# Optimization experiments

Measured on AMD Instinct MI355X. Metric: run time of the kernel, lower is better.

## Reference

```python
import jax, jax.numpy as jnp
import numpy as np

D_MODEL = 512
N_LAYERS = 4
VOCAB = 256
SEQ = 2048
BATCH = 8
EPS = 1e-5


def _ln(x, g, b):
    mu = jnp.mean(x, axis=-1, keepdims=True)
    var = jnp.mean(jnp.square(x - mu), axis=-1, keepdims=True)
    return (x - mu) * jax.lax.rsqrt(var + EPS) * g + b


def setup_inputs() -> dict:
    key = jax.random.key(0)
    ks = jax.random.split(key, 16)
    d, dff = D_MODEL, 4 * D_MODEL
    s = 0.02
    inp = {
        "tokens": jax.random.randint(ks[0], (BATCH, SEQ), 0, VOCAB, dtype=jnp.int64),
        "emb": jax.random.normal(ks[1], (VOCAB, d), jnp.float32) * s,
        "W_upd": jax.random.normal(ks[2], (d, d), jnp.float32) * s,
        "b_upd": jnp.zeros((d,), jnp.float32),
        "W_f": jax.random.normal(ks[3], (d, d), jnp.float32) * s,
        "b_f": jnp.zeros((d,), jnp.float32),
        "decay_param": jnp.zeros((1,), jnp.float32),
        "norm_g": jnp.ones((d,), jnp.float32),
        "norm_b": jnp.zeros((d,), jnp.float32),
        "cms_ln_g": jnp.ones((N_LAYERS, d), jnp.float32),
        "cms_ln_b": jnp.zeros((N_LAYERS, d), jnp.float32),
        "cms_W1": jax.random.normal(ks[4], (N_LAYERS, d, dff), jnp.float32) * s,
        "cms_b1": jnp.zeros((N_LAYERS, dff), jnp.float32),
        "cms_W2": jax.random.normal(ks[5], (N_LAYERS, dff, d), jnp.float32) * s,
        "cms_b2": jnp.zeros((N_LAYERS, d), jnp.float32),
        "head_W": jax.random.normal(ks[6], (d, VOCAB), jnp.float32) * s,
        "head_b": jnp.zeros((VOCAB,), jnp.float32),
    }
    return inp


def _fast_memory(x, mask, W_upd, b_upd, W_f, b_f, decay_param):
    # x: (B,S,d), mask: (B,S) float
    decay = jax.nn.sigmoid(decay_param[0])
    u = jnp.einsum("bsd,de->bse", x, W_upd) + b_upd  # precompute updates
    u_t = jnp.swapaxes(u, 0, 1)                        # (S,B,d)
    m_t = jnp.swapaxes(mask, 0, 1)[..., None]          # (S,B,1)

    def step(mem, inp):
        u_i, msk = inp
        new = decay * mem + u_i
        mem = msk * new + (1.0 - msk) * mem
        return mem, mem

    mem0 = jnp.zeros((x.shape[0], x.shape[2]), x.dtype)
    _, mems = jax.lax.scan(step, mem0, (u_t, m_t))     # (S,B,d)
    mems = jnp.swapaxes(mems, 0, 1)                    # (B,S,d)
    return jnp.einsum("bsd,de->bse", mems, W_f) + b_f


def reference(tokens, emb, W_upd, b_upd, W_f, b_f, decay_param, norm_g, norm_b,
              cms_ln_g, cms_ln_b, cms_W1, cms_b1, cms_W2, cms_b2, head_W, head_b):
    mask = (tokens != 0).astype(emb.dtype)
    x = emb[tokens]                                    # (B,S,d)
    x = x + _fast_memory(x, mask, W_upd, b_upd, W_f, b_f, decay_param)
    x = _ln(x, norm_g, norm_b)
    for i in range(N_LAYERS):
        h = _ln(x, cms_ln_g[i], cms_ln_b[i])
        h = jax.nn.gelu(jnp.einsum("bsd,df->bsf", h, cms_W1[i]) + cms_b1[i], approximate=False)
        h = jnp.einsum("bsf,fd->bsd", h, cms_W2[i]) + cms_b2[i]
        x = x + h
    return jnp.einsum("bsd,dv->bsv", x, head_W) + head_b
```

## Files before the change

### kernel.cpp

```cpp
#include <hip/hip_runtime.h>
#include <hip/hip_bf16.h>
#include <math.h>

#define D_MODEL 512
#define N_LAYERS 4
#define SEQ 2048
#define BATCH 8
#define M_TOT (BATCH * SEQ)
#define DFF 2048
#define HEAD_V 256
#define SC 32
#define NC (SEQ / SC)

typedef __hip_bfloat16 bf16;
typedef __bf16 bf16x8 __attribute__((ext_vector_type(8)));
typedef float f32x4 __attribute__((ext_vector_type(4)));

__device__ __forceinline__ unsigned short bfbits(float x) {
    bf16 h = __float2bfloat16(x);
    return *(unsigned short*)&h;
}
__device__ __forceinline__ unsigned int pk(float a, float b) {
    return (unsigned int)bfbits(a) | ((unsigned int)bfbits(b) << 16);
}

__device__ __forceinline__ float gelu_f(float x) {
    float t2 = 1.5957691216f * (x + 0.044715f * x * x * x);
    float e = __expf(t2);
    return x - x * __builtin_amdgcn_rcpf(e + 1.0f);
}

__global__ void convT_kernel(const float* __restrict__ W, bf16* __restrict__ WT,
                             int R, int C, size_t wstride, size_t tstride) {
    W += (size_t)blockIdx.z * wstride;
    WT += (size_t)blockIdx.z * tstride;
    __shared__ float t[32][33];
    int r0 = blockIdx.x * 32, c0 = blockIdx.y * 32;
    int tx = threadIdx.x, ty = threadIdx.y;
    #pragma unroll
    for (int i = 0; i < 32; i += 8)
        t[ty + i][tx] = W[(size_t)(r0 + ty + i) * C + c0 + tx];
    __syncthreads();
    #pragma unroll
    for (int i = 0; i < 32; i += 8)
        WT[(size_t)(c0 + ty + i) * R + r0 + tx] = __float2bfloat16(t[tx][ty + i]);
}

__global__ void embed_kernel(const int* __restrict__ tokens,
                             const float* __restrict__ emb,
                             float* __restrict__ xf, bf16* __restrict__ xb) {
    int row = blockIdx.x, t = threadIdx.x;
    int tok = tokens[row];
    float4 v = ((const float4*)(emb + (size_t)tok * D_MODEL))[t];
    ((float4*)(xf + (size_t)row * D_MODEL))[t] = v;
    uint2 st; st.x = pk(v.x, v.y); st.y = pk(v.z, v.w);
    ((uint2*)(xb + (size_t)row * D_MODEL))[t] = st;
}

__global__ void scanA_kernel(bf16* __restrict__ u, const int* __restrict__ tokens,
                             const float* __restrict__ decayp,
                             float* __restrict__ L, float* __restrict__ P) {
    int idx = blockIdx.x;
    int dblk = idx & 1;
    int c = (idx >> 1) & (NC - 1);
    int b = idx >> 7;
    int d = dblk * 256 + threadIdx.x;
    float decay = 1.0f / (1.0f + __expf(-decayp[0]));
    const int* tok = tokens + (size_t)b * SEQ + c * SC;
    bf16* up = u + ((size_t)b * SEQ + (size_t)c * SC) * D_MODEL + d;
    float mem = 0.0f;
    #pragma unroll 4
    for (int s = 0; s < SC; ++s) {
        float ui = __bfloat162float(up[(size_t)s * D_MODEL]);
        bool m = (tok[s] != 0);
        mem = (m ? decay : 1.0f) * mem + (m ? ui : 0.0f);
        up[(size_t)s * D_MODEL] = __float2bfloat16(mem);
    }
    L[((size_t)b * NC + c) * D_MODEL + d] = mem;
    if (threadIdx.x == 0 && dblk == 0) {
        int cnt = 0;
        for (int s = 0; s < SC; ++s) cnt += (tok[s] != 0);
        P[b * NC + c] = __powf(decay, (float)cnt);
    }
}

__global__ void scanB_kernel(const float* __restrict__ L, const float* __restrict__ P,
                             float* __restrict__ Mc) {
    int b = blockIdx.x >> 1;
    int d = (blockIdx.x & 1) * 256 + threadIdx.x;
    float carry = 0.0f;
    for (int c = 0; c < NC; ++c) {
        size_t off = ((size_t)b * NC + c) * D_MODEL + d;
        Mc[off] = carry;
        carry = P[b * NC + c] * carry + L[off];
    }
}

__global__ void scanC_kernel(bf16* __restrict__ u, const int* __restrict__ tokens,
                             const float* __restrict__ decayp,
                             const float* __restrict__ Mc) {
    int idx = blockIdx.x;
    int dblk = idx & 1;
    int c = (idx >> 1) & (NC - 1);
    int b = idx >> 7;
    if (c == 0) return;
    int d = dblk * 256 + threadIdx.x;
    float decay = 1.0f / (1.0f + __expf(-decayp[0]));
    const int* tok = tokens + (size_t)b * SEQ + c * SC;
    bf16* up = u + ((size_t)b * SEQ + (size_t)c * SC) * D_MODEL + d;
    float carry = Mc[((size_t)b * NC + c) * D_MODEL + d];
    float coeff = 1.0f;
    #pragma unroll 4
    for (int s = 0; s < SC; ++s) {
        bool m = (tok[s] != 0);
        coeff *= (m ? decay : 1.0f);
        float local = __bfloat162float(up[(size_t)s * D_MODEL]);
        up[(size_t)s * D_MODEL] = __float2bfloat16(local + carry * coeff);
    }
}

__device__ __forceinline__ void ln_body(const float* __restrict__ in,
                                        float* __restrict__ outf,
                                        bf16* __restrict__ outb,
                                        const float* __restrict__ g,
                                        const float* __restrict__ b,
                                        int WF, int WB) {
    int w = threadIdx.x >> 6, lane = threadIdx.x & 63;
    int row = blockIdx.x * 4 + w;
    const float4* ip = (const float4*)(in + (size_t)row * D_MODEL);
    float4 v0 = ip[lane * 2], v1 = ip[lane * 2 + 1];
    float s1 = v0.x + v0.y + v0.z + v0.w + v1.x + v1.y + v1.z + v1.w;
    float s2 = v0.x * v0.x + v0.y * v0.y + v0.z * v0.z + v0.w * v0.w +
               v1.x * v1.x + v1.y * v1.y + v1.z * v1.z + v1.w * v1.w;
    #pragma unroll
    for (int off = 32; off; off >>= 1) {
        s1 += __shfl_xor(s1, off);
        s2 += __shfl_xor(s2, off);
    }
    float mu = s1 * (1.0f / D_MODEL);
    float var = s2 * (1.0f / D_MODEL) - mu * mu;
    float rstd = rsqrtf(var + 1e-5f);
    const float4* g4 = (const float4*)g;
    const float4* b4 = (const float4*)b;
    float4 g0 = g4[lane * 2], g1 = g4[lane * 2 + 1];
    float4 b0 = b4[lane * 2], b1 = b4[lane * 2 + 1];
    float4 o0, o1;
    o0.x = (v0.x - mu) * rstd * g0.x + b0.x;
    o0.y = (v0.y - mu) * rstd * g0.y + b0.y;
    o0.z = (v0.z - mu) * rstd * g0.z + b0.z;
    o0.w = (v0.w - mu) * rstd * g0.w + b0.w;
    o1.x = (v1.x - mu) * rstd * g1.x + b1.x;
    o1.y = (v1.y - mu) * rstd * g1.y + b1.y;
    o1.z = (v1.z - mu) * rstd * g1.z + b1.z;
    o1.w = (v1.w - mu) * rstd * g1.w + b1.w;
    if (WF) {
        float4* op = (float4*)(outf + (size_t)row * D_MODEL);
        op[lane * 2] = o0; op[lane * 2 + 1] = o1;
    }
    if (WB) {
        uint4 st;
        st.x = pk(o0.x, o0.y); st.y = pk(o0.z, o0.w);
        st.z = pk(o1.x, o1.y); st.w = pk(o1.z, o1.w);
        ((uint4*)(outb + (size_t)row * D_MODEL))[lane] = st;
    }
}

__global__ void ln_f32_kernel(const float* __restrict__ in, float* __restrict__ outf,
                              const float* __restrict__ g, const float* __restrict__ b) {
    ln_body(in, outf, nullptr, g, b, 1, 0);
}
__global__ void ln_b16_kernel(const float* __restrict__ in, bf16* __restrict__ outb,
                              const float* __restrict__ g, const float* __restrict__ b) {
    ln_body(in, nullptr, outb, g, b, 0, 1);
}

#define STAGE(buf, k0)                                                        \
    do {                                                                      \
        _Pragma("unroll")                                                     \
        for (int it = 0; it < AIT; ++it) {                                    \
            int cc = tid + it * 512;                                          \
            int l = cc ^ ((cc >> 3) & 7);                                     \
            __builtin_amdgcn_global_load_lds(                                 \
                A + (size_t)(m0 + l / CHR) * K + (k0) + (l % CHR) * 8,        \
                smem + (buf) * TILEB + cc * 16, 16, 0, 0);                    \
        }                                                                     \
        _Pragma("unroll")                                                     \
        for (int it = 0; it < BIT; ++it) {                                    \
            int cc = tid + it * 512;                                          \
            int l = cc ^ ((cc >> 3) & 7);                                     \
            __builtin_amdgcn_global_load_lds(                                 \
                BT + (size_t)(n0 + l / CHR) * K + (k0) + (l % CHR) * 8,       \
                smem + (buf) * TILEB + BM * BK * 2 + cc * 16, 16, 0, 0);      \
        }                                                                     \
    } while (0)

template <int BMODE, int GELU, int RES, int OBF>
__device__ __forceinline__ void gemm_body(char* smem,
                          const bf16* __restrict__ A, const bf16* __restrict__ BT,
                          const float* __restrict__ bias, const float* __restrict__ R,
                          float* __restrict__ Cf, bf16* __restrict__ Cb,
                          int N, int K) {
    constexpr int BM = BMODE ? 128 : 256;
    constexpr int BK = BMODE ? 64 : 32;
    constexpr int WM = BM / 2;
    constexpr int MI = WM / 16;
    constexpr int KS = BK / 32;
    constexpr int CHR = BK / 8;
    constexpr int AIT = BM * BK * 2 / 16 / 512;
    constexpr int BIT = 256 * BK * 2 / 16 / 512;
    constexpr int TILEB = (BM + 256) * BK * 2;
    constexpr int ST = 68;
    const int tid = threadIdx.x;
    const int lane = tid & 63;
    const int w = tid >> 6;
    const int wr = w >> 2, wc = w & 3;
    const int lm = lane & 15, lk = lane >> 4;
    const int swz = BMODE ? ((lm & 7) << 4) : (((lm >> 1) & 7) << 4);
    const int m0 = blockIdx.x * BM, n0 = blockIdx.y * 256;

    f32x4 acc[MI][4] = {};
    const int nt = K / BK;

    STAGE(0, 0);
    STAGE(1, BK);
    int cur = 0;
    for (int t = 0; t < nt; ++t) {
        if (t + 2 < nt) {
            int nb = cur + 2; if (nb >= 3) nb -= 3;
            STAGE(nb, (t + 2) * BK);
            if constexpr (BMODE == 0) asm volatile("s_waitcnt vmcnt(8)" ::: "memory");
            else                      asm volatile("s_waitcnt vmcnt(12)" ::: "memory");
        } else if (t + 1 < nt) {
            if constexpr (BMODE == 0) asm volatile("s_waitcnt vmcnt(4)" ::: "memory");
            else                      asm volatile("s_waitcnt vmcnt(6)" ::: "memory");
        } else {
            asm volatile("s_waitcnt vmcnt(0)" ::: "memory");
        }
        __builtin_amdgcn_s_barrier();
        __builtin_amdgcn_sched_barrier(0);
        const char* Ab = smem + cur * TILEB;
        const char* Bb = Ab + BM * BK * 2;
        #pragma unroll
        for (int ks = 0; ks < KS; ++ks) {
            bf16x8 fb[4];
            #pragma unroll
            for (int nf = 0; nf < 4; ++nf) {
                int boff = (wc * 64 + nf * 16 + lm) * BK * 2 + ks * 64 + lk * 16;
                fb[nf] = *(const bf16x8*)(Bb + (boff ^ swz));
            }
            #pragma unroll
            for (int mh = 0; mh < MI / 4; ++mh) {
                bf16x8 fa[4];
                #pragma unroll
                for (int mf = 0; mf < 4; ++mf) {
                    int aoff = (wr * WM + (mh * 4 + mf) * 16 + lm) * BK * 2 + ks * 64 + lk * 16;
                    fa[mf] = *(const bf16x8*)(Ab + (aoff ^ swz));
                }
                __builtin_amdgcn_s_setprio(1);
                #pragma unroll
                for (int mf = 0; mf < 4; ++mf)
                    #pragma unroll
                    for (int nf = 0; nf < 4; ++nf)
                        acc[mh * 4 + mf][nf] = __builtin_amdgcn_mfma_f32_16x16x32_bf16(
                            fa[mf], fb[nf], acc[mh * 4 + mf][nf], 0, 0, 0);
                __builtin_amdgcn_s_setprio(0);
            }
        }
        __builtin_amdgcn_s_barrier();
        cur = (cur == 2) ? 0 : cur + 1;
    }
    __syncthreads();

    float* ep = (float*)smem + w * 16 * ST;
    const int r2 = lane >> 2;
    const int q = lane & 3;
    const int gc0 = n0 + wc * 64 + q * 16;
    #pragma unroll
    for (int i = 0; i < MI; ++i) {
        #pragma unroll
        for (int nf = 0; nf < 4; ++nf)
            #pragma unroll
            for (int r = 0; r < 4; ++r)
                ep[(lk * 4 + r) * ST + nf * 16 + lm] = acc[i][nf][r];
        int grow = m0 + wr * WM + i * 16 + r2;
        float4 fx[4];
        #pragma unroll
        for (int v = 0; v < 4; ++v)
            fx[v] = *(const float4*)&ep[r2 * ST + q * 16 + v * 4];
        #pragma unroll
        for (int v = 0; v < 4; ++v) {
            float4 bb = *(const float4*)(bias + gc0 + v * 4);
            fx[v].x += bb.x; fx[v].y += bb.y; fx[v].z += bb.z; fx[v].w += bb.w;
            if (GELU) {
                fx[v].x = gelu_f(fx[v].x);
                fx[v].y = gelu_f(fx[v].y);
                fx[v].z = gelu_f(fx[v].z);
                fx[v].w = gelu_f(fx[v].w);
            }
            if (RES) {
                float4 rr = *(const float4*)(R + (size_t)grow * N + gc0 + v * 4);
                fx[v].x += rr.x; fx[v].y += rr.y; fx[v].z += rr.z; fx[v].w += rr.w;
            }
        }
        if (OBF == 0 || OBF == 2) {
            #pragma unroll
            for (int v = 0; v < 4; ++v)
                *(float4*)(Cf + (size_t)grow * N + gc0 + v * 4) = fx[v];
        }
        if (OBF >= 1) {
            uint4 s1, s2;
            s1.x = pk(fx[0].x, fx[0].y); s1.y = pk(fx[0].z, fx[0].w);
            s1.z = pk(fx[1].x, fx[1].y); s1.w = pk(fx[1].z, fx[1].w);
            s2.x = pk(fx[2].x, fx[2].y); s2.y = pk(fx[2].z, fx[2].w);
            s2.z = pk(fx[3].x, fx[3].y); s2.w = pk(fx[3].z, fx[3].w);
            *(uint4*)(Cb + (size_t)grow * N + gc0) = s1;
            *(uint4*)(Cb + (size_t)grow * N + gc0 + 8) = s2;
        }
    }
}

#define DEF_GEMM(name, BMODE, GELU, RES, OBF)                                 \
__launch_bounds__(512) __global__ void name(                                  \
        const bf16* __restrict__ A, const bf16* __restrict__ BT,              \
        const float* __restrict__ bias, const float* __restrict__ R,          \
        float* __restrict__ Cf, bf16* __restrict__ Cb, int N, int K) {        \
    __shared__ char smem[3 * (((BMODE) ? 128 : 256) + 256) * ((BMODE) ? 64 : 32) * 2]; \
    gemm_body<BMODE, GELU, RES, OBF>(smem, A, BT, bias, R, Cf, Cb, N, K);     \
}

DEF_GEMM(gemm_gelu,    0, 1, 0, 1)
DEF_GEMM(gemm_u,       1, 0, 0, 1)
DEF_GEMM(gemm_res,     1, 0, 1, 0)
DEF_GEMM(gemm_resboth, 1, 0, 1, 2)
DEF_GEMM(gemm_plain,   1, 0, 0, 0)

extern "C" void kernel_launch(void* const* d_in, const int* in_sizes, int n_in,
                              void* d_out, int out_size, void* d_ws, size_t ws_size,
                              hipStream_t stream) {
    const int*   tokens = (const int*)d_in[0];
    const float* emb    = (const float*)d_in[1];
    const float* W_upd  = (const float*)d_in[2];
    const float* b_upd  = (const float*)d_in[3];
    const float* W_f    = (const float*)d_in[4];
    const float* b_f    = (const float*)d_in[5];
    const float* decayp = (const float*)d_in[6];
    const float* norm_g = (const float*)d_in[7];
    const float* norm_b = (const float*)d_in[8];
    const float* cms_g  = (const float*)d_in[9];
    const float* cms_b  = (const float*)d_in[10];
    const float* cW1    = (const float*)d_in[11];
    const float* cb1    = (const float*)d_in[12];
    const float* cW2    = (const float*)d_in[13];
    const float* cb2    = (const float*)d_in[14];
    const float* head_W = (const float*)d_in[15];
    const float* head_b = (const float*)d_in[16];
    float* out = (float*)d_out;

    const int M = M_TOT, D = D_MODEL, F = DFF, V = HEAD_V;

    float* xf = (float*)d_ws;
    bf16*  lnb = (bf16*)((char*)d_ws + (size_t)M * D * 4);
    bf16*  wb  = (bf16*)((char*)lnb + (size_t)M * D * 2);
    const size_t WB_ELEMS = 9043968;
    char* dyn = (char*)wb + WB_ELEMS * 2;
    size_t used = (size_t)(dyn - (char*)d_ws);
    size_t avail = ws_size > used ? ws_size - used : 0;
    int MC = 4096;
    if (avail >= (size_t)16384 * F * 2) MC = 16384;
    else if (avail >= (size_t)8192 * F * 2) MC = 8192;
    bf16* ub = (bf16*)dyn;
    bf16* hb = (bf16*)dyn;

    float* scanL = out;
    float* scanM = out + (size_t)BATCH * NC * D;
    float* scanP = scanM + (size_t)BATCH * NC * D;

    bf16* WupdT = wb;
    bf16* WfT   = wb + 262144;
    bf16* W1T   = wb + 524288;
    bf16* W2T   = wb + 4718592;
    bf16* HWT   = wb + 8912896;

    dim3 tb(32, 8);
    convT_kernel<<<dim3(16, 16, 2), tb, 0, stream>>>(W_upd, WupdT, D, D,
                                                     (size_t)(W_f - W_upd), 262144);
    convT_kernel<<<dim3(16, 64, N_LAYERS), tb, 0, stream>>>(cW1, W1T, D, F,
                                                            (size_t)D * F, 1048576);
    convT_kernel<<<dim3(64, 16, N_LAYERS), tb, 0, stream>>>(cW2, W2T, F, D,
                                                            (size_t)F * D, 1048576);
    convT_kernel<<<dim3(16, 8, 1), tb, 0, stream>>>(head_W, HWT, D, V, 0, 0);

    embed_kernel<<<M, 128, 0, stream>>>(tokens, emb, xf, lnb);

    gemm_u<<<dim3(M / 128, D / 256), 512, 0, stream>>>(
        lnb, WupdT, b_upd, nullptr, nullptr, ub, D, D);
    scanA_kernel<<<BATCH * NC * 2, 256, 0, stream>>>(ub, tokens, decayp, scanL, scanP);
    scanB_kernel<<<BATCH * 2, 256, 0, stream>>>(scanL, scanP, scanM);
    scanC_kernel<<<BATCH * NC * 2, 256, 0, stream>>>(ub, tokens, decayp, scanM);
    gemm_res<<<dim3(M / 128, D / 256), 512, 0, stream>>>(
        ub, WfT, b_f, xf, xf, nullptr, D, D);
    ln_f32_kernel<<<M / 4, 256, 0, stream>>>(xf, xf, norm_g, norm_b);

    for (int l = 0; l < N_LAYERS; ++l) {
        ln_b16_kernel<<<M / 4, 256, 0, stream>>>(xf, lnb,
                                                 cms_g + (size_t)l * D,
                                                 cms_b + (size_t)l * D);
        bool last = (l == N_LAYERS - 1);
        for (int mc = 0; mc < M; mc += MC) {
            gemm_gelu<<<dim3(MC / 256, F / 256), 512, 0, stream>>>(
                lnb + (size_t)mc * D, W1T + (size_t)l * 1048576,
                cb1 + (size_t)l * F, nullptr, nullptr, hb, F, D);
            if (last)
                gemm_resboth<<<dim3(MC / 128, D / 256), 512, 0, stream>>>(
                    hb, W2T + (size_t)l * 1048576, cb2 + (size_t)l * D,
                    xf + (size_t)mc * D, xf + (size_t)mc * D,
                    lnb + (size_t)mc * D, D, F);
            else
                gemm_res<<<dim3(MC / 128, D / 256), 512, 0, stream>>>(
                    hb, W2T + (size_t)l * 1048576, cb2 + (size_t)l * D,
                    xf + (size_t)mc * D, xf + (size_t)mc * D, nullptr, D, F);
        }
    }

    gemm_plain<<<dim3(M / 128, V / 256), 512, 0, stream>>>(
        lnb, HWT, head_b, nullptr, out, nullptr, V, D);
}
```

Baseline: 557.5 us.

## Shrink GEMM tiles, switch to double buffering, raise occupancy hint

Halves the M tile of every GEMM variant: 256 to 128 for the GELU GEMM and 128 to 64 for the rest. The three-stage LDS ring becomes a two-stage ping-pong with matching vmcnt waits, and launch bounds now ask for 4 blocks per CU. The goal is more blocks in flight and less LDS per block, so occupancy and load balance improve across the CUs. The cost is lower per-block data reuse, more redundant B-tile loads, a shallower prefetch pipeline, and a register cap that may cause spills.

```diff
diff --git a/kernel.cpp b/kernel.cpp
--- a/kernel.cpp
+++ b/kernel.cpp
@@ -194,20 +194,19 @@
         }                                                                     \
     } while (0)
 
-template <int BMODE, int GELU, int RES, int OBF>
+template <int BM, int BK, int GELU, int RES, int OBF>
 __device__ __forceinline__ void gemm_body(char* smem,
                           const bf16* __restrict__ A, const bf16* __restrict__ BT,
                           const float* __restrict__ bias, const float* __restrict__ R,
                           float* __restrict__ Cf, bf16* __restrict__ Cb,
                           int N, int K) {
-    constexpr int BM = BMODE ? 128 : 256;
-    constexpr int BK = BMODE ? 64 : 32;
     constexpr int WM = BM / 2;
     constexpr int MI = WM / 16;
     constexpr int KS = BK / 32;
     constexpr int CHR = BK / 8;
-    constexpr int AIT = BM * BK * 2 / 16 / 512;
-    constexpr int BIT = 256 * BK * 2 / 16 / 512;
+    constexpr int AIT = BM * BK / 4096;
+    constexpr int BIT = 256 * BK / 4096;
+    constexpr int SL = AIT + BIT;
     constexpr int TILEB = (BM + 256) * BK * 2;
     constexpr int ST = 68;
     const int tid = threadIdx.x;
@@ -215,24 +214,19 @@
     const int w = tid >> 6;
     const int wr = w >> 2, wc = w & 3;
     const int lm = lane & 15, lk = lane >> 4;
-    const int swz = BMODE ? ((lm & 7) << 4) : (((lm >> 1) & 7) << 4);
+    const int swz = (BK == 64) ? ((lm & 7) << 4) : (((lm >> 1) & 7) << 4);
     const int m0 = blockIdx.x * BM, n0 = blockIdx.y * 256;
 
     f32x4 acc[MI][4] = {};
     const int nt = K / BK;
 
     STAGE(0, 0);
-    STAGE(1, BK);
     int cur = 0;
     for (int t = 0; t < nt; ++t) {
-        if (t + 2 < nt) {
-            int nb = cur + 2; if (nb >= 3) nb -= 3;
-            STAGE(nb, (t + 2) * BK);
-            if constexpr (BMODE == 0) asm volatile("s_waitcnt vmcnt(8)" ::: "memory");
-            else                      asm volatile("s_waitcnt vmcnt(12)" ::: "memory");
-        } else if (t + 1 < nt) {
-            if constexpr (BMODE == 0) asm volatile("s_waitcnt vmcnt(4)" ::: "memory");
-            else                      asm volatile("s_waitcnt vmcnt(6)" ::: "memory");
+        if (t + 1 < nt) {
+            STAGE(cur ^ 1, (t + 1) * BK);
+            if constexpr (SL == 3) asm volatile("s_waitcnt vmcnt(3)" ::: "memory");
+            else                   asm volatile("s_waitcnt vmcnt(5)" ::: "memory");
         } else {
             asm volatile("s_waitcnt vmcnt(0)" ::: "memory");
         }
@@ -242,32 +236,28 @@
         const char* Bb = Ab + BM * BK * 2;
         #pragma unroll
         for (int ks = 0; ks < KS; ++ks) {
-            bf16x8 fb[4];
+            bf16x8 fa[MI], fb[4];
             #pragma unroll
             for (int nf = 0; nf < 4; ++nf) {
                 int boff = (wc * 64 + nf * 16 + lm) * BK * 2 + ks * 64 + lk * 16;
                 fb[nf] = *(const bf16x8*)(Bb + (boff ^ swz));
             }
             #pragma unroll
-            for (int mh = 0; mh < MI / 4; ++mh) {
-                bf16x8 fa[4];
+            for (int mf = 0; mf < MI; ++mf) {
+                int aoff = (wr * WM + mf * 16 + lm) * BK * 2 + ks * 64 + lk * 16;
+                fa[mf] = *(const bf16x8*)(Ab + (aoff ^ swz));
+            }
+            __builtin_amdgcn_s_setprio(1);
+            #pragma unroll
+            for (int mf = 0; mf < MI; ++mf)
                 #pragma unroll
-                for (int mf = 0; mf < 4; ++mf) {
-                    int aoff = (wr * WM + (mh * 4 + mf) * 16 + lm) * BK * 2 + ks * 64 + lk * 16;
-                    fa[mf] = *(const bf16x8*)(Ab + (aoff ^ swz));
-                }
-                __builtin_amdgcn_s_setprio(1);
-                #pragma unroll
-                for (int mf = 0; mf < 4; ++mf)
-                    #pragma unroll
-                    for (int nf = 0; nf < 4; ++nf)
-                        acc[mh * 4 + mf][nf] = __builtin_amdgcn_mfma_f32_16x16x32_bf16(
-                            fa[mf], fb[nf], acc[mh * 4 + mf][nf], 0, 0, 0);
-                __builtin_amdgcn_s_setprio(0);
-            }
+                for (int nf = 0; nf < 4; ++nf)
+                    acc[mf][nf] = __builtin_amdgcn_mfma_f32_16x16x32_bf16(
+                        fa[mf], fb[nf], acc[mf][nf], 0, 0, 0);
+            __builtin_amdgcn_s_setprio(0);
         }
         __builtin_amdgcn_s_barrier();
-        cur = (cur == 2) ? 0 : cur + 1;
+        cur ^= 1;
     }
     __syncthreads();
 
@@ -319,20 +309,20 @@
     }
 }
 
-#define DEF_GEMM(name, BMODE, GELU, RES, OBF)                                 \
-__launch_bounds__(512) __global__ void name(                                  \
+#define DEF_GEMM(name, BM, BK, GELU, RES, OBF)                                \
+__launch_bounds__(512, 4) __global__ void name(                               \
         const bf16* __restrict__ A, const bf16* __restrict__ BT,              \
         const float* __restrict__ bias, const float* __restrict__ R,          \
         float* __restrict__ Cf, bf16* __restrict__ Cb, int N, int K) {        \
-    __shared__ char smem[3 * (((BMODE) ? 128 : 256) + 256) * ((BMODE) ? 64 : 32) * 2]; \
-    gemm_body<BMODE, GELU, RES, OBF>(smem, A, BT, bias, R, Cf, Cb, N, K);     \
-}
-
-DEF_GEMM(gemm_gelu,    0, 1, 0, 1)
-DEF_GEMM(gemm_u,       1, 0, 0, 1)
-DEF_GEMM(gemm_res,     1, 0, 1, 0)
-DEF_GEMM(gemm_resboth, 1, 0, 1, 2)
-DEF_GEMM(gemm_plain,   1, 0, 0, 0)
+    __shared__ char smem[2 * ((BM) + 256) * (BK) * 2];                        \
+    gemm_body<BM, BK, GELU, RES, OBF>(smem, A, BT, bias, R, Cf, Cb, N, K);    \
+}
+
+DEF_GEMM(gemm_gelu,    128, 32, 1, 0, 1)
+DEF_GEMM(gemm_u,        64, 64, 0, 0, 1)
+DEF_GEMM(gemm_res,      64, 64, 0, 1, 0)
+DEF_GEMM(gemm_resboth,  64, 64, 0, 1, 2)
+DEF_GEMM(gemm_plain,    64, 64, 0, 0, 0)
 
 extern "C" void kernel_launch(void* const* d_in, const int* in_sizes, int n_in,
                               void* d_out, int out_size, void* d_ws, size_t ws_size,
@@ -392,12 +382,12 @@
 
     embed_kernel<<<M, 128, 0, stream>>>(tokens, emb, xf, lnb);
 
-    gemm_u<<<dim3(M / 128, D / 256), 512, 0, stream>>>(
+    gemm_u<<<dim3(M / 64, D / 256), 512, 0, stream>>>(
         lnb, WupdT, b_upd, nullptr, nullptr, ub, D, D);
     scanA_kernel<<<BATCH * NC * 2, 256, 0, stream>>>(ub, tokens, decayp, scanL, scanP);
     scanB_kernel<<<BATCH * 2, 256, 0, stream>>>(scanL, scanP, scanM);
     scanC_kernel<<<BATCH * NC * 2, 256, 0, stream>>>(ub, tokens, decayp, scanM);
-    gemm_res<<<dim3(M / 128, D / 256), 512, 0, stream>>>(
+    gemm_res<<<dim3(M / 64, D / 256), 512, 0, stream>>>(
         ub, WfT, b_f, xf, xf, nullptr, D, D);
     ln_f32_kernel<<<M / 4, 256, 0, stream>>>(xf, xf, norm_g, norm_b);
 
@@ -407,21 +397,21 @@
                                                  cms_b + (size_t)l * D);
         bool last = (l == N_LAYERS - 1);
         for (int mc = 0; mc < M; mc += MC) {
-            gemm_gelu<<<dim3(MC / 256, F / 256), 512, 0, stream>>>(
+            gemm_gelu<<<dim3(MC / 128, F / 256), 512, 0, stream>>>(
                 lnb + (size_t)mc * D, W1T + (size_t)l * 1048576,
                 cb1 + (size_t)l * F, nullptr, nullptr, hb, F, D);
             if (last)
-                gemm_resboth<<<dim3(MC / 128, D / 256), 512, 0, stream>>>(
+                gemm_resboth<<<dim3(MC / 64, D / 256), 512, 0, stream>>>(
                     hb, W2T + (size_t)l * 1048576, cb2 + (size_t)l * D,
                     xf + (size_t)mc * D, xf + (size_t)mc * D,
                     lnb + (size_t)mc * D, D, F);
             else
-                gemm_res<<<dim3(MC / 128, D / 256), 512, 0, stream>>>(
+                gemm_res<<<dim3(MC / 64, D / 256), 512, 0, stream>>>(
                     hb, W2T + (size_t)l * 1048576, cb2 + (size_t)l * D,
                     xf + (size_t)mc * D, xf + (size_t)mc * D, nullptr, D, F);
         }
     }
 
-    gemm_plain<<<dim3(M / 128, V / 256), 512, 0, stream>>>(
+    gemm_plain<<<dim3(M / 64, V / 256), 512, 0, stream>>>(
         lnb, HWT, head_b, nullptr, out, nullptr, V, D);
 }
```

Measured after the change: 548.1 us. No clear change (-1.7%).
